# Kernel optimization log

Hardware: AMD Instinct MI355X
Metric: run time of the kernel (lower is better)

## Reference

```python
import jax, jax.numpy as jnp
import numpy as np

DN = ("NCHW", "OIHW", "NCHW")


def _conv(x, w, b, pad):
    y = jax.lax.conv_general_dilated(x, w, (1, 1), ((pad, pad), (pad, pad)), dimension_numbers=DN)
    return y + b[None, :, None, None]


def _deconv(x, w, b):
    # torch ConvTranspose2d(k=4, s=2, p=1); w: [I, O, 4, 4]
    w_eff = jnp.transpose(w, (1, 0, 2, 3))[:, :, ::-1, ::-1]  # OIHW, rot180
    y = jax.lax.conv_general_dilated(x, w_eff, (1, 1), ((2, 2), (2, 2)), lhs_dilation=(2, 2), dimension_numbers=DN)
    return y + b[None, :, None, None]


def setup_inputs() -> dict:
    key = jax.random.key(0)
    ks = jax.random.split(key, 8)
    C, Cs, H, Hs, K = 256, 768, 256, 8, 2048
    rn = lambda k, shape, scale: jax.random.normal(k, shape, jnp.float32) * scale
    return {
        "down": rn(ks[0], (1, C, H, H), 1.0),
        "swint": rn(ks[1], (1, Cs, Hs, Hs), 1.0),
        "wt_w": rn(ks[2], (C, Cs, 1, 1), 1.0 / np.sqrt(Cs)),
        "wt_b": jnp.zeros((C,), jnp.float32),
        "up_dw": rn(ks[3], (5, C, C, 4, 4), 1.0 / np.sqrt(C * 16)),
        "up_db": jnp.zeros((5, C), jnp.float32),
        "up_cw": rn(ks[4], (5, C, C, 3, 3), 1.0 / np.sqrt(C * 9)),
        "up_cb": jnp.zeros((5, C), jnp.float32),
        "gate_w": rn(ks[5], (1, C, 1, 1), 1.0 / np.sqrt(C)),
        "gate_b": jnp.zeros((1,), jnp.float32),
        "in_w": rn(ks[6], (3 * C, C), 1.0 / np.sqrt(C)),
        "in_b": jnp.zeros((3 * C,), jnp.float32),
        "out_w": rn(ks[7], (C, C), 1.0 / np.sqrt(C)),
        "out_b": jnp.zeros((C,), jnp.float32),
        "k": K,
    }


def reference(down, swint, wt_w, wt_b, up_dw, up_db, up_cw, up_cb, gate_w, gate_b, in_w, in_b, out_w, out_b, k):
    NH = 8
    B, C, H, W = down.shape  # B == 1
    s = _conv(swint, wt_w, wt_b, 0)
    for i in range(up_dw.shape[0]):
        s = _conv(jax.nn.relu(_deconv(s, up_dw[i], up_db[i])), up_cw[i], up_cb[i], 1)
    gate = jax.nn.sigmoid(_conv(down, gate_w, gate_b, 0))  # [1,1,H,W]
    down_flat = down[0].reshape(C, H * W).T  # [HW, C]
    s_flat = s[0].reshape(C, H * W).T        # [HW, C]
    _, idx = jax.lax.top_k(gate.reshape(-1), k)  # [k]
    q_in = down_flat[idx]   # [k, C]
    kv_in = s_flat[idx]     # [k, C]
    # MultiheadAttention (seq-first, batch 1)
    qw, kw, vw = in_w[:C], in_w[C:2 * C], in_w[2 * C:]
    qb, kb, vb = in_b[:C], in_b[C:2 * C], in_b[2 * C:]
    hd = C // NH
    q = (q_in @ qw.T + qb).reshape(k, NH, hd)
    kk = (kv_in @ kw.T + kb).reshape(k, NH, hd)
    v = (kv_in @ vw.T + vb).reshape(k, NH, hd)
    scores = jnp.einsum("qhd,khd->hqk", q, kk) / jnp.sqrt(jnp.asarray(hd, q.dtype))
    attn = jax.nn.softmax(scores, axis=-1)
    o = jnp.einsum("hqk,khd->qhd", attn, v).reshape(k, C)
    o = o @ out_w.T + out_b
    # scatter attended subset back into full feature map
    attended = down_flat.at[idx].set(o)
    return attended.T.reshape(B, C, H, W)
```

## Files before the change

kernel.cpp:

```cpp
#include <hip/hip_runtime.h>
#include <math.h>

#define CCH 256
#define HWP 65536
#define PCI 40

typedef short short8 __attribute__((ext_vector_type(8)));
typedef float f32x4 __attribute__((ext_vector_type(4)));
typedef unsigned short us4 __attribute__((ext_vector_type(4)));

__device__ inline unsigned short f2bf(float f) {
  unsigned u = __float_as_uint(f);
  return (unsigned short)((u + 0x7FFFu + ((u >> 16) & 1u)) >> 16);
}
__device__ inline float bf2f(unsigned short s) {
  return __uint_as_float(((unsigned)s) << 16);
}

__device__ inline void mfma_bf16(f32x4& d, short8 a, short8 b) {
  asm volatile("v_mfma_f32_16x16x32_bf16 %0, %1, %2, %0" : "+v"(d) : "v"(a), "v"(b));
}

static const size_t BUF_B_OFF = 67108864;
static const size_t TAIL_OFF  = 134217728;
static const size_t KEYS_OFF  = TAIL_OFF;
static const size_t HIST_OFF  = TAIL_OFF + 262144;
static const size_t STATE_OFF = TAIL_OFF + 263168;
static const size_t IDX_OFF   = TAIL_OFF + 263424;
static const size_t EQ_OFF    = TAIL_OFF + 271616;
static const size_t OB_OFF    = 6291456;
static const size_t WBI_OFF   = 8388608;
static const size_t WBO_OFF   = 9437184;
static const size_t SROWS_OFF = 10485760;
static const size_t DQ_OFF    = 12582912;
static const size_t GPART_OFF = 16777216;
static const size_t WT5_OFF   = 20971520;
static const size_t QB_OFF    = 31457280;
static const size_t KB_OFF    = 32505856;
static const size_t VT_OFF    = 33554432;
static const size_t CPK_OFF   = 37748736;
static const size_t DPK_OFF   = 44040192;
static const size_t WTW_OFF   = 54525952;
static const size_t WPART_OFF = 55050240;
static const size_t XQ0_OFF   = 57671680;

struct SelState { unsigned int P; int kneed; int nGreater; int nEqual; };

__global__ void k_init(unsigned int* hist, SelState* st) {
  int t = threadIdx.x;
  hist[t] = 0;
  if (t == 0) { st->P = 0u; st->kneed = 2048; st->nGreater = 0; st->nEqual = 0; }
}

__global__ void k_packall(const float* __restrict__ up_cw, const float* __restrict__ up_dw,
                          const float* __restrict__ in_w, const float* __restrict__ out_w,
                          const float* __restrict__ wt_w,
                          short* __restrict__ cpk, short* __restrict__ dpk,
                          short* __restrict__ wB5, short* __restrict__ wBi,
                          short* __restrict__ wBo, short* __restrict__ wBt) {
  int b = blockIdx.x;
  int tid = threadIdx.x;
  if (b < 1024) {
    int layer = b >> 8, co = b & 255, ci = tid;
    const float* wl = up_cw + (size_t)layer * 589824;
    short* wo = cpk + (size_t)layer * 589824;
    for (int tap = 0; tap < 9; ++tap)
      wo[((size_t)(tap * 256 + co) * 256) + ci] = (short)f2bf(wl[((size_t)(co * 256 + ci)) * 9 + tap]);
  } else if (b < 2304) {
    int bb = b - 1024;
    int layer = bb >> 8, co = bb & 255, ci = tid;
    const float* wl = up_dw + (size_t)layer * 1048576;
    for (int pq = 0; pq < 4; ++pq) {
      int p = pq >> 1, q = pq & 1;
      for (int tt = 0; tt < 4; ++tt) {
        int dyi = tt >> 1, dxi = tt & 1;
        int wr = dyi ? (1 - p) : (3 - p);
        int wc = dxi ? (1 - q) : (3 - q);
        dpk[((size_t)layer * 1048576) + ((size_t)((pq * 4 + tt) * 256 + co) * 256) + ci] =
            (short)f2bf(wl[((size_t)(ci * 256 + co)) * 16 + wr * 4 + wc]);
      }
    }
  } else if (b < 2560) {
    int co = b - 2304;
    const float* w5 = up_cw + 2359296;
    for (int kk = tid; kk < 2304; kk += 256) {
      int c = kk / 288, r = kk % 288;
      int e = r >> 5, cl = r & 31;
      wB5[(size_t)co * 2304 + kk] = (short)f2bf(w5[(size_t)co * 2304 + (size_t)(c * 32 + cl) * 9 + e]);
    }
  } else if (b < 3328) {
    int o = b - 2560;
    wBi[(size_t)o * 256 + tid] = (short)f2bf(in_w[(size_t)o * 256 + tid]);
  } else if (b < 3584) {
    int o = b - 3328;
    wBo[(size_t)o * 256 + tid] = (short)f2bf(out_w[(size_t)o * 256 + tid]);
  } else {
    int co = b - 3584;
    for (int kk = tid; kk < 768; kk += 256)
      wBt[(size_t)co * 768 + kk] = (short)f2bf(wt_w[(size_t)co * 768 + kk]);
  }
}

__global__ void k_gatecopy2(const float* __restrict__ down, const float* __restrict__ gw,
                            float* __restrict__ out, float* __restrict__ gpart) {
  int p = blockIdx.x * 256 + threadIdx.x;
  int cc = blockIdx.y;
  float acc = 0.f;
  for (int c = cc * 32; c < cc * 32 + 32; ++c) {
    float v = down[(size_t)c * HWP + p];
    out[(size_t)c * HWP + p] = v;
    acc += v * gw[c];
  }
  gpart[(size_t)cc * HWP + p] = acc;
}

__global__ void k_gkey(const float* __restrict__ gpart, unsigned* __restrict__ keys) {
  int p = blockIdx.x * 256 + threadIdx.x;
  float s = 0.f;
  for (int cc = 0; cc < 8; ++cc) s += gpart[(size_t)cc * HWP + p];
  unsigned u = __float_as_uint(s);
  keys[p] = (u & 0x80000000u) ? ~u : (u | 0x80000000u);
}

__global__ void k_hist(const unsigned int* __restrict__ keys, unsigned int* hist,
                       const SelState* st, int r) {
  __shared__ unsigned int lh[256];
  int t = threadIdx.x;
  lh[t] = 0;
  __syncthreads();
  unsigned int key = keys[blockIdx.x * 256 + t];
  bool ok = (r == 0) || ((key >> (32 - 8 * r)) == st->P);
  if (ok) atomicAdd(&lh[(key >> (24 - 8 * r)) & 255u], 1u);
  __syncthreads();
  if (lh[t]) atomicAdd(&hist[t], lh[t]);
}

__global__ void k_scan(unsigned int* hist, SelState* st) {
  if (threadIdx.x == 0) {
    int need = st->kneed;
    unsigned int cum = 0;
    for (int b = 255; b >= 0; --b) {
      unsigned int h = hist[b];
      if (cum + h >= (unsigned int)need) {
        st->P = (st->P << 8) | (unsigned int)b;
        st->kneed = need - (int)cum;
        break;
      }
      cum += h;
    }
  }
  __syncthreads();
  hist[threadIdx.x] = 0;
}

__global__ void k_compact(const unsigned int* __restrict__ keys, SelState* st,
                          int* __restrict__ idx, int* __restrict__ eq) {
  int p = blockIdx.x * 256 + threadIdx.x;
  unsigned int key = keys[p];
  unsigned int P = st->P;
  if (key > P) {
    int pos = atomicAdd(&st->nGreater, 1);
    idx[pos] = p;
  } else if (key == P) {
    int e = atomicAdd(&st->nEqual, 1);
    if (e < 4096) eq[e] = p;
  }
}

__global__ void k_finalize(SelState* st, int* idx, int* eq) {
  if (threadIdx.x != 0) return;
  int n = st->nEqual;
  if (n > 4096) n = 4096;
  for (int i = 1; i < n; ++i) {
    int v = eq[i], j = i - 1;
    while (j >= 0 && eq[j] > v) { eq[j + 1] = eq[j]; --j; }
    eq[j + 1] = v;
  }
  int g = st->nGreater;
  for (int i = 0; i < st->kneed; ++i) idx[g + i] = eq[i];
}

__global__ void k_gatherq(const float* __restrict__ down, const int* __restrict__ idx,
                          short* __restrict__ dq) {
  int j = blockIdx.x, c = threadIdx.x;
  int p = idx[j];
  dq[(size_t)j * 256 + c] = (short)f2bf(down[(size_t)c * HWP + p]);
}

__global__ __launch_bounds__(256) void k_wtconvP(const float* __restrict__ swint,
                                                 const short* __restrict__ wBt,
                                                 float* __restrict__ wpart) {
  __shared__ short x_s[64 * 40];
  int t = threadIdx.x, l = t & 63, wv = t >> 6;
  int co0 = blockIdx.x * 64;
  int ks = blockIdx.y;
  int kbase = ks * 96;
  f32x4 acc[4];
#pragma unroll
  for (int m = 0; m < 4; ++m) { f32x4 z = {0.f, 0.f, 0.f, 0.f}; acc[m] = z; }
#pragma unroll
  for (int cc = 0; cc < 3; ++cc) {
    int c0 = kbase + cc * 32;
    __syncthreads();
    {
      int ci = t >> 3, pos0 = (t & 7) * 8;
      const float* sp = swint + (size_t)(c0 + ci) * 64 + pos0;
#pragma unroll
      for (int pp = 0; pp < 8; ++pp)
        x_s[(pos0 + pp) * 40 + ci] = (short)f2bf(sp[pp]);
    }
    __syncthreads();
    short8 bfrag = *(const short8*)&x_s[(wv * 16 + (l & 15)) * 40 + (l >> 4) * 8];
#pragma unroll
    for (int m = 0; m < 4; ++m) {
      short8 af = *(const short8*)&wBt[(size_t)(co0 + m * 16 + (l & 15)) * 768 + c0 + (l >> 4) * 8];
      mfma_bf16(acc[m], af, bfrag);
    }
  }
  asm volatile("s_nop 7\n\ts_nop 7" ::);
  int pos = wv * 16 + (l & 15);
#pragma unroll
  for (int m = 0; m < 4; ++m)
#pragma unroll
    for (int r = 0; r < 4; ++r) {
      int co = co0 + m * 16 + (l >> 4) * 4 + r;
      wpart[((size_t)ks * 64 + pos) * 256 + co] = acc[m][r];
    }
}

__global__ void k_wtred(const float* __restrict__ wpart, const float* __restrict__ bias,
                        short* __restrict__ xq0) {
  int pos = blockIdx.x, co = threadIdx.x;
  float s = bias[co];
  for (int ks = 0; ks < 8; ++ks) s += wpart[((size_t)ks * 64 + pos) * 256 + co];
  xq0[(size_t)pos * 256 + co] = (short)f2bf(s);
}

__global__ __launch_bounds__(256) void k_deconv8M(const short* __restrict__ xq0,
                                                  const short* __restrict__ wpk,
                                                  const float* __restrict__ bias,
                                                  unsigned* __restrict__ yp) {
  __shared__ short x_s[121 * 260];
  int t = threadIdx.x, l = t & 63, wv = t >> 6;
  int co0 = blockIdx.x * 64;
  int pq = blockIdx.y, p = pq >> 1, q = pq & 1;
  const unsigned* xs32 = (const unsigned*)xq0;
  for (int i = t; i < 121 * 128; i += 256) {
    int row = i >> 7, c2 = i & 127;
    int iy = row / 11 - 1, ix = row % 11 - 1;
    unsigned v = 0;
    if (iy >= 0 && iy < 8 && ix >= 0 && ix < 8)
      v = xs32[(size_t)(iy * 8 + ix) * 128 + c2];
    *(unsigned*)&x_s[row * 260 + 2 * c2] = v;
  }
  __syncthreads();
  f32x4 acc[4];
#pragma unroll
  for (int m = 0; m < 4; ++m) { f32x4 z = {0.f, 0.f, 0.f, 0.f}; acc[m] = z; }
  int pos = wv * 16 + (l & 15);
  int ay = pos >> 3, bx = pos & 7;
#pragma unroll
  for (int tt = 0; tt < 4; ++tt) {
    int dyi = tt >> 1, dxi = tt & 1;
    int rowx = (ay + p + dyi) * 11 + (bx + q + dxi);
#pragma unroll
    for (int c0 = 0; c0 < 256; c0 += 32) {
      short8 bfrag = *(const short8*)&x_s[rowx * 260 + c0 + (l >> 4) * 8];
#pragma unroll
      for (int m = 0; m < 4; ++m) {
        short8 af = *(const short8*)&wpk[((size_t)((pq * 4 + tt) * 256 + co0 + m * 16 + (l & 15)) * 256) + c0 + (l >> 4) * 8];
        mfma_bf16(acc[m], af, bfrag);
      }
    }
  }
  asm volatile("s_nop 7\n\ts_nop 7" ::);
  int oy = 2 * ay + p, ox = 2 * bx + q;
#pragma unroll
  for (int m = 0; m < 4; ++m)
#pragma unroll
    for (int r4p = 0; r4p < 2; ++r4p) {
      int cob = co0 + m * 16 + (l >> 4) * 4 + 2 * r4p;
      unsigned pk = (unsigned)f2bf(fmaxf(acc[m][2 * r4p] + bias[cob], 0.f))
                  | ((unsigned)f2bf(fmaxf(acc[m][2 * r4p + 1] + bias[cob + 1], 0.f)) << 16);
      yp[(size_t)(cob >> 1) * 256 + oy * 16 + ox] = pk;
    }
}

template <int S, int O>
__global__ __launch_bounds__(256) void k_conv3u(const unsigned* __restrict__ xp,
                                                const short* __restrict__ wpk,
                                                const float* __restrict__ bias,
                                                unsigned* __restrict__ yp) {
  constexpr int WPC = (S >= 64) ? 2 : 1;
  constexpr int WCO = 4 / WPC;
  constexpr int COS = 64 / WCO;
  constexpr int MR = COS / 16;
  constexpr int PSP = S / WPC;
  constexpr int NR = PSP / 16;
  constexpr int CBK = (S + 2 + 31) / 32;
  constexpr int RS = O + 2;
  __shared__ short x_s[RS * (S + 2) * PCI];
  unsigned* x_s32 = (unsigned*)x_s;
  int t = threadIdx.x, l = t & 63, wv = t >> 6;
  int wcob = (wv % WCO) * COS;
  int wposb = (wv / WCO) * PSP;
  int row0 = blockIdx.x * O;
  int co0 = blockIdx.y * 64;
  int colb = t & 31, ci2b = t >> 5;
  f32x4 acc[O][MR][NR];
#pragma unroll
  for (int o = 0; o < O; ++o)
#pragma unroll
    for (int m = 0; m < MR; ++m)
#pragma unroll
      for (int n = 0; n < NR; ++n) { f32x4 z = {0.f, 0.f, 0.f, 0.f}; acc[o][m][n] = z; }
  for (int c0 = 0; c0 < CCH; c0 += 32) {
    int cb = c0 >> 1;
    __syncthreads();
#pragma unroll
    for (int r = 0; r < RS; ++r) {
      int gy = row0 - 1 + r;
      bool yok = (gy >= 0 && gy < S);
#pragma unroll
      for (int cbk = 0; cbk < CBK; ++cbk) {
        int col = colb + cbk * 32;
        if (col < S + 2) {
          int gx = col - 1;
          bool ok = yok && (gx >= 0) && (gx < S);
          unsigned v0 = 0, v1 = 0;
          if (ok) {
            size_t gbase = (size_t)(cb + ci2b) * S * S + (size_t)gy * S + gx;
            v0 = xp[gbase];
            v1 = xp[gbase + (size_t)8 * S * S];
          }
          int lb = (r * (S + 2) + col) * (PCI / 2);
          x_s32[lb + ci2b] = v0;
          x_s32[lb + ci2b + 8] = v1;
        }
      }
    }
    __syncthreads();
#pragma unroll
    for (int dyg = 0; dyg < 3; ++dyg)
#pragma unroll
      for (int dx = 0; dx < 3; ++dx) {
        short8 a[MR];
#pragma unroll
        for (int m = 0; m < MR; ++m)
          a[m] = *(const short8*)&wpk[((size_t)((dyg * 3 + dx) * 256 + co0 + wcob + m * 16 + (l & 15)) * 256) + c0 + (l >> 4) * 8];
#pragma unroll
        for (int o = 0; o < O; ++o) {
          short8 b[NR];
#pragma unroll
          for (int n = 0; n < NR; ++n)
            b[n] = *(const short8*)&x_s[((dyg + o) * (S + 2) + wposb + n * 16 + (l & 15) + dx) * PCI + (l >> 4) * 8];
#pragma unroll
          for (int m = 0; m < MR; ++m)
#pragma unroll
            for (int n = 0; n < NR; ++n) mfma_bf16(acc[o][m][n], a[m], b[n]);
        }
      }
  }
  asm volatile("s_nop 7\n\ts_nop 7" ::);
#pragma unroll
  for (int o = 0; o < O; ++o)
#pragma unroll
    for (int m = 0; m < MR; ++m)
#pragma unroll
      for (int n = 0; n < NR; ++n) {
        int cob = co0 + wcob + m * 16 + (l >> 4) * 4;
        int px = wposb + n * 16 + (l & 15);
#pragma unroll
        for (int r4p = 0; r4p < 2; ++r4p) {
          unsigned pk = (unsigned)f2bf(acc[o][m][n][2 * r4p] + bias[cob + 2 * r4p])
                      | ((unsigned)f2bf(acc[o][m][n][2 * r4p + 1] + bias[cob + 2 * r4p + 1]) << 16);
          yp[(size_t)((cob >> 1) + r4p) * S * S + (size_t)(row0 + o) * S + px] = pk;
        }
      }
}

__global__ __launch_bounds__(512) void k_conv3v(const unsigned* __restrict__ xp,
                                                const short* __restrict__ wpk,
                                                const float* __restrict__ bias,
                                                unsigned* __restrict__ yp) {
  constexpr int S = 128;
  constexpr int MR = 2;
  constexpr int PSP = 32;
  constexpr int NR = 2;
  __shared__ short x_s[3 * (S + 2) * PCI];
  __shared__ short w_s[9 * 64 * PCI];
  unsigned* x_s32 = (unsigned*)x_s;
  int t = threadIdx.x, l = t & 63, wv = t >> 6;
  int wcob = (wv & 1) * 32;
  int wposb = (wv >> 1) * PSP;
  int row0 = blockIdx.x;
  int co0 = blockIdx.y * 64;
  int colb = t & 31, ci2b = t >> 5;
  f32x4 acc[MR][NR];
#pragma unroll
  for (int m = 0; m < MR; ++m)
#pragma unroll
    for (int n = 0; n < NR; ++n) { f32x4 z = {0.f, 0.f, 0.f, 0.f}; acc[m][n] = z; }
  for (int c0 = 0; c0 < CCH; c0 += 32) {
    int cb = c0 >> 1;
    __syncthreads();
#pragma unroll
    for (int r = 0; r < 3; ++r) {
      int gy = row0 - 1 + r;
      bool yok = (gy >= 0 && gy < S);
#pragma unroll
      for (int cbk = 0; cbk < 5; ++cbk) {
        int col = colb + cbk * 32;
        if (col < S + 2) {
          int gx = col - 1;
          bool ok = yok && (gx >= 0) && (gx < S);
          unsigned v = 0;
          if (ok)
            v = xp[(size_t)(cb + ci2b) * S * S + (size_t)gy * S + gx];
          x_s32[(r * (S + 2) + col) * (PCI / 2) + ci2b] = v;
        }
      }
    }
    for (int i = t; i < 4608; i += 512) {
      int seg8 = i & 7;
      int rowi = i >> 3;
      int tap = rowi >> 6, co = rowi & 63;
      us4 wv4 = *(const us4*)&wpk[((size_t)(tap * 256 + co0 + co) * 256) + c0 + seg8 * 4];
      *(us4*)&w_s[rowi * PCI + seg8 * 4] = wv4;
    }
    __syncthreads();
#pragma unroll
    for (int dyg = 0; dyg < 3; ++dyg)
#pragma unroll
      for (int dx = 0; dx < 3; ++dx) {
        short8 a[MR];
#pragma unroll
        for (int m = 0; m < MR; ++m)
          a[m] = *(const short8*)&w_s[((dyg * 3 + dx) * 64 + wcob + m * 16 + (l & 15)) * PCI + (l >> 4) * 8];
        short8 b[NR];
#pragma unroll
        for (int n = 0; n < NR; ++n)
          b[n] = *(const short8*)&x_s[(dyg * (S + 2) + wposb + n * 16 + (l & 15) + dx) * PCI + (l >> 4) * 8];
#pragma unroll
        for (int m = 0; m < MR; ++m)
#pragma unroll
          for (int n = 0; n < NR; ++n) mfma_bf16(acc[m][n], a[m], b[n]);
      }
  }
  asm volatile("s_nop 7\n\ts_nop 7" ::);
#pragma unroll
  for (int m = 0; m < MR; ++m)
#pragma unroll
    for (int n = 0; n < NR; ++n) {
      int cob = co0 + wcob + m * 16 + (l >> 4) * 4;
      int px = wposb + n * 16 + (l & 15);
#pragma unroll
      for (int r4p = 0; r4p < 2; ++r4p) {
        unsigned pk = (unsigned)f2bf(acc[m][n][2 * r4p] + bias[cob + 2 * r4p])
                    | ((unsigned)f2bf(acc[m][n][2 * r4p + 1] + bias[cob + 2 * r4p + 1]) << 16);
        yp[(size_t)((cob >> 1) + r4p) * S * S + (size_t)row0 * S + px] = pk;
      }
    }
}

__global__ __launch_bounds__(512) void k_conv3v64(const unsigned* __restrict__ xp,
                                                  const short* __restrict__ wpk,
                                                  const float* __restrict__ bias,
                                                  unsigned* __restrict__ yp) {
  constexpr int S = 64;
  constexpr int MR = 2;
  __shared__ short x_s[3 * (S + 2) * PCI];
  __shared__ short w_s[9 * 64 * PCI];
  unsigned* x_s32 = (unsigned*)x_s;
  int t = threadIdx.x, l = t & 63, wv = t >> 6;
  int wcob = (wv & 1) * 32;
  int wposb = (wv >> 1) * 16;
  int row0 = blockIdx.x;
  int co0 = blockIdx.y * 64;
  int colb = t & 31, ci2b = t >> 5;
  f32x4 acc[MR];
#pragma unroll
  for (int m = 0; m < MR; ++m) { f32x4 z = {0.f, 0.f, 0.f, 0.f}; acc[m] = z; }
  for (int c0 = 0; c0 < CCH; c0 += 32) {
    int cb = c0 >> 1;
    __syncthreads();
#pragma unroll
    for (int r = 0; r < 3; ++r) {
      int gy = row0 - 1 + r;
      bool yok = (gy >= 0 && gy < S);
#pragma unroll
      for (int cbk = 0; cbk < 3; ++cbk) {
        int col = colb + cbk * 32;
        if (col < S + 2) {
          int gx = col - 1;
          bool ok = yok && (gx >= 0) && (gx < S);
          unsigned v = 0;
          if (ok)
            v = xp[(size_t)(cb + ci2b) * S * S + (size_t)gy * S + gx];
          x_s32[(r * (S + 2) + col) * (PCI / 2) + ci2b] = v;
        }
      }
    }
    for (int i = t; i < 4608; i += 512) {
      int seg8 = i & 7;
      int rowi = i >> 3;
      int tap = rowi >> 6, co = rowi & 63;
      us4 wv4 = *(const us4*)&wpk[((size_t)(tap * 256 + co0 + co) * 256) + c0 + seg8 * 4];
      *(us4*)&w_s[rowi * PCI + seg8 * 4] = wv4;
    }
    __syncthreads();
#pragma unroll
    for (int dyg = 0; dyg < 3; ++dyg)
#pragma unroll
      for (int dx = 0; dx < 3; ++dx) {
        short8 a[MR];
#pragma unroll
        for (int m = 0; m < MR; ++m)
          a[m] = *(const short8*)&w_s[((dyg * 3 + dx) * 64 + wcob + m * 16 + (l & 15)) * PCI + (l >> 4) * 8];
        short8 b = *(const short8*)&x_s[(dyg * (S + 2) + wposb + (l & 15) + dx) * PCI + (l >> 4) * 8];
#pragma unroll
        for (int m = 0; m < MR; ++m) mfma_bf16(acc[m], a[m], b);
      }
  }
  asm volatile("s_nop 7\n\ts_nop 7" ::);
#pragma unroll
  for (int m = 0; m < MR; ++m) {
    int cob = co0 + wcob + m * 16 + (l >> 4) * 4;
    int px = wposb + (l & 15);
#pragma unroll
    for (int r4p = 0; r4p < 2; ++r4p) {
      unsigned pk = (unsigned)f2bf(acc[m][2 * r4p] + bias[cob + 2 * r4p])
                  | ((unsigned)f2bf(acc[m][2 * r4p + 1] + bias[cob + 2 * r4p + 1]) << 16);
      yp[(size_t)((cob >> 1) + r4p) * S * S + (size_t)row0 * S + px] = pk;
    }
  }
}

template <int S, int O>
__global__ __launch_bounds__(256) void k_deconvu(const unsigned* __restrict__ xp,
                                                 const short* __restrict__ wpk,
                                                 const float* __restrict__ bias,
                                                 unsigned* __restrict__ yp) {
  constexpr int WPC = (S >= 64) ? 2 : 1;
  constexpr int WCO = 4 / WPC;
  constexpr int COS = 64 / WCO;
  constexpr int MR = COS / 16;
  constexpr int PSP = S / WPC;
  constexpr int NR = PSP / 16;
  constexpr int CBK = (S + 2 + 31) / 32;
  constexpr int RS = O + 1;
  const int SO = 2 * S;
  __shared__ short x_s[RS * (S + 2) * PCI];
  __shared__ short w_s[8 * 64 * PCI];
  unsigned* x_s32 = (unsigned*)x_s;
  int t = threadIdx.x, l = t & 63, wv = t >> 6;
  int wcob = (wv % WCO) * COS;
  int wposb = (wv / WCO) * PSP;
  int row0 = blockIdx.x * O;
  int co0 = blockIdx.y * 64;
  int p = blockIdx.z;
  int colb = t & 31, ci2b = t >> 5;
  f32x4 acc[2][O][MR][NR];
#pragma unroll
  for (int q = 0; q < 2; ++q)
#pragma unroll
    for (int o = 0; o < O; ++o)
#pragma unroll
      for (int m = 0; m < MR; ++m)
#pragma unroll
        for (int n = 0; n < NR; ++n) { f32x4 z = {0.f, 0.f, 0.f, 0.f}; acc[q][o][m][n] = z; }
  for (int c0 = 0; c0 < CCH; c0 += 32) {
    int cb = c0 >> 1;
    __syncthreads();
#pragma unroll
    for (int r = 0; r < RS; ++r) {
      int gy = row0 + p - 1 + r;
      bool yok = (gy >= 0 && gy < S);
#pragma unroll
      for (int cbk = 0; cbk < CBK; ++cbk) {
        int col = colb + cbk * 32;
        if (col < S + 2) {
          int gx = col - 1;
          bool ok = yok && (gx >= 0) && (gx < S);
          unsigned v0 = 0, v1 = 0;
          if (ok) {
            size_t gbase = (size_t)(cb + ci2b) * S * S + (size_t)gy * S + gx;
            v0 = xp[gbase];
            v1 = xp[gbase + (size_t)8 * S * S];
          }
          int lb = (r * (S + 2) + col) * (PCI / 2);
          x_s32[lb + ci2b] = v0;
          x_s32[lb + ci2b + 8] = v1;
        }
      }
    }
    for (int i = t; i < 4096; i += 256) {
      int seg8 = i & 7;
      int rowi = i >> 3;
      int c8 = rowi >> 6, co = rowi & 63;
      int qq = c8 >> 2, tt = c8 & 3;
      us4 wv4 = *(const us4*)&wpk[((size_t)(((2 * p + qq) * 4 + tt) * 256 + co0 + co) * 256) + c0 + seg8 * 4];
      *(us4*)&w_s[rowi * PCI + seg8 * 4] = wv4;
    }
    __syncthreads();
#pragma unroll
    for (int dyi = 0; dyi < 2; ++dyi)
#pragma unroll
      for (int o = 0; o < O; ++o) {
        short8 b[3][NR];
#pragma unroll
        for (int off = 0; off < 3; ++off)
#pragma unroll
          for (int n = 0; n < NR; ++n)
            b[off][n] = *(const short8*)&x_s[((dyi + o) * (S + 2) + wposb + n * 16 + (l & 15) + off) * PCI + (l >> 4) * 8];
#pragma unroll
        for (int q = 0; q < 2; ++q)
#pragma unroll
          for (int dxi = 0; dxi < 2; ++dxi) {
            int c8 = q * 4 + dyi * 2 + dxi;
            short8 a[MR];
#pragma unroll
            for (int m = 0; m < MR; ++m)
              a[m] = *(const short8*)&w_s[(c8 * 64 + wcob + m * 16 + (l & 15)) * PCI + (l >> 4) * 8];
#pragma unroll
            for (int m = 0; m < MR; ++m)
#pragma unroll
              for (int n = 0; n < NR; ++n) mfma_bf16(acc[q][o][m][n], a[m], b[dxi + q][n]);
          }
      }
  }
  asm volatile("s_nop 7\n\ts_nop 7" ::);
#pragma unroll
  for (int o = 0; o < O; ++o) {
    int oy = 2 * (row0 + o) + p;
#pragma unroll
    for (int m = 0; m < MR; ++m)
#pragma unroll
      for (int n = 0; n < NR; ++n) {
        int px = wposb + n * 16 + (l & 15);
#pragma unroll
        for (int r4p = 0; r4p < 2; ++r4p) {
          int cob = co0 + wcob + m * 16 + (l >> 4) * 4 + 2 * r4p;
          float b0 = bias[cob], b1 = bias[cob + 1];
          unsigned pk0 = (unsigned)f2bf(fmaxf(acc[0][o][m][n][2 * r4p] + b0, 0.f))
                       | ((unsigned)f2bf(fmaxf(acc[0][o][m][n][2 * r4p + 1] + b1, 0.f)) << 16);
          unsigned pk1 = (unsigned)f2bf(fmaxf(acc[1][o][m][n][2 * r4p] + b0, 0.f))
                       | ((unsigned)f2bf(fmaxf(acc[1][o][m][n][2 * r4p + 1] + b1, 0.f)) << 16);
          uint2 pk = make_uint2(pk0, pk1);
          *(uint2*)&yp[(size_t)(cob >> 1) * SO * SO + (size_t)oy * SO + 2 * px] = pk;
        }
      }
  }
}

__global__ __launch_bounds__(512) void k_deconvw(const unsigned* __restrict__ xp,
                                                 const short* __restrict__ wpk,
                                                 const float* __restrict__ bias,
                                                 unsigned* __restrict__ yp) {
  constexpr int S = 128;
  constexpr int O = 2;
  constexpr int MR = 2;
  constexpr int PSP = 32;
  constexpr int NR = 2;
  constexpr int RS = O + 1;
  const int SO = 2 * S;
  __shared__ short x_s[RS * (S + 2) * PCI];
  __shared__ short w_s[8 * 64 * PCI];
  unsigned* x_s32 = (unsigned*)x_s;
  int t = threadIdx.x, l = t & 63, wv = t >> 6;
  int wcob = (wv & 1) * 32;
  int wposb = (wv >> 1) * PSP;
  int row0 = blockIdx.x * O;
  int co0 = blockIdx.y * 64;
  int p = blockIdx.z;
  int colb = t & 31, ci2b = t >> 5;
  f32x4 acc[2][O][MR][NR];
#pragma unroll
  for (int q = 0; q < 2; ++q)
#pragma unroll
    for (int o = 0; o < O; ++o)
#pragma unroll
      for (int m = 0; m < MR; ++m)
#pragma unroll
        for (int n = 0; n < NR; ++n) { f32x4 z = {0.f, 0.f, 0.f, 0.f}; acc[q][o][m][n] = z; }
  for (int c0 = 0; c0 < CCH; c0 += 32) {
    int cb = c0 >> 1;
    __syncthreads();
#pragma unroll
    for (int r = 0; r < RS; ++r) {
      int gy = row0 + p - 1 + r;
      bool yok = (gy >= 0 && gy < S);
#pragma unroll
      for (int cbk = 0; cbk < 5; ++cbk) {
        int col = colb + cbk * 32;
        if (col < S + 2) {
          int gx = col - 1;
          bool ok = yok && (gx >= 0) && (gx < S);
          unsigned v = 0;
          if (ok)
            v = xp[(size_t)(cb + ci2b) * S * S + (size_t)gy * S + gx];
          x_s32[(r * (S + 2) + col) * (PCI / 2) + ci2b] = v;
        }
      }
    }
    for (int i = t; i < 4096; i += 512) {
      int seg8 = i & 7;
      int rowi = i >> 3;
      int c8 = rowi >> 6, co = rowi & 63;
      int qq = c8 >> 2, tt = c8 & 3;
      us4 wv4 = *(const us4*)&wpk[((size_t)(((2 * p + qq) * 4 + tt) * 256 + co0 + co) * 256) + c0 + seg8 * 4];
      *(us4*)&w_s[rowi * PCI + seg8 * 4] = wv4;
    }
    __syncthreads();
#pragma unroll
    for (int dyi = 0; dyi < 2; ++dyi)
#pragma unroll
      for (int o = 0; o < O; ++o) {
        short8 b[3][NR];
#pragma unroll
        for (int off = 0; off < 3; ++off)
#pragma unroll
          for (int n = 0; n < NR; ++n)
            b[off][n] = *(const short8*)&x_s[((dyi + o) * (S + 2) + wposb + n * 16 + (l & 15) + off) * PCI + (l >> 4) * 8];
#pragma unroll
        for (int q = 0; q < 2; ++q)
#pragma unroll
          for (int dxi = 0; dxi < 2; ++dxi) {
            int c8 = q * 4 + dyi * 2 + dxi;
            short8 a[MR];
#pragma unroll
            for (int m = 0; m < MR; ++m)
              a[m] = *(const short8*)&w_s[(c8 * 64 + wcob + m * 16 + (l & 15)) * PCI + (l >> 4) * 8];
#pragma unroll
            for (int m = 0; m < MR; ++m)
#pragma unroll
              for (int n = 0; n < NR; ++n) mfma_bf16(acc[q][o][m][n], a[m], b[dxi + q][n]);
          }
      }
  }
  asm volatile("s_nop 7\n\ts_nop 7" ::);
#pragma unroll
  for (int o = 0; o < O; ++o) {
    int oy = 2 * (row0 + o) + p;
#pragma unroll
    for (int m = 0; m < MR; ++m)
#pragma unroll
      for (int n = 0; n < NR; ++n) {
        int px = wposb + n * 16 + (l & 15);
#pragma unroll
        for (int r4p = 0; r4p < 2; ++r4p) {
          int cob = co0 + wcob + m * 16 + (l >> 4) * 4 + 2 * r4p;
          float b0 = bias[cob], b1 = bias[cob + 1];
          unsigned pk0 = (unsigned)f2bf(fmaxf(acc[0][o][m][n][2 * r4p] + b0, 0.f))
                       | ((unsigned)f2bf(fmaxf(acc[0][o][m][n][2 * r4p + 1] + b1, 0.f)) << 16);
          unsigned pk1 = (unsigned)f2bf(fmaxf(acc[1][o][m][n][2 * r4p] + b0, 0.f))
                       | ((unsigned)f2bf(fmaxf(acc[1][o][m][n][2 * r4p + 1] + b1, 0.f)) << 16);
          uint2 pk = make_uint2(pk0, pk1);
          *(uint2*)&yp[(size_t)(cob >> 1) * SO * SO + (size_t)oy * SO + 2 * px] = pk;
        }
      }
  }
}

__global__ __launch_bounds__(512) void k_deconvw64(const unsigned* __restrict__ xp,
                                                   const short* __restrict__ wpk,
                                                   const float* __restrict__ bias,
                                                   unsigned* __restrict__ yp) {
  constexpr int S = 64;
  constexpr int MR = 2;
  const int SO = 2 * S;
  __shared__ short x_s[2 * (S + 2) * PCI];
  __shared__ short w_s[8 * 64 * PCI];
  unsigned* x_s32 = (unsigned*)x_s;
  int t = threadIdx.x, l = t & 63, wv = t >> 6;
  int wcob = (wv & 1) * 32;
  int wposb = (wv >> 1) * 16;
  int row0 = blockIdx.x;
  int co0 = blockIdx.y * 64;
  int p = blockIdx.z;
  int colb = t & 31, ci2b = t >> 5;
  f32x4 acc[2][MR];
#pragma unroll
  for (int q = 0; q < 2; ++q)
#pragma unroll
    for (int m = 0; m < MR; ++m) { f32x4 z = {0.f, 0.f, 0.f, 0.f}; acc[q][m] = z; }
  for (int c0 = 0; c0 < CCH; c0 += 32) {
    int cb = c0 >> 1;
    __syncthreads();
#pragma unroll
    for (int r = 0; r < 2; ++r) {
      int gy = row0 + p - 1 + r;
      bool yok = (gy >= 0 && gy < S);
#pragma unroll
      for (int cbk = 0; cbk < 3; ++cbk) {
        int col = colb + cbk * 32;
        if (col < S + 2) {
          int gx = col - 1;
          bool ok = yok && (gx >= 0) && (gx < S);
          unsigned v = 0;
          if (ok)
            v = xp[(size_t)(cb + ci2b) * S * S + (size_t)gy * S + gx];
          x_s32[(r * (S + 2) + col) * (PCI / 2) + ci2b] = v;
        }
      }
    }
    for (int i = t; i < 4096; i += 512) {
      int seg8 = i & 7;
      int rowi = i >> 3;
      int c8 = rowi >> 6, co = rowi & 63;
      int qq = c8 >> 2, tt = c8 & 3;
      us4 wv4 = *(const us4*)&wpk[((size_t)(((2 * p + qq) * 4 + tt) * 256 + co0 + co) * 256) + c0 + seg8 * 4];
      *(us4*)&w_s[rowi * PCI + seg8 * 4] = wv4;
    }
    __syncthreads();
#pragma unroll
    for (int dyi = 0; dyi < 2; ++dyi) {
      short8 b[3];
#pragma unroll
      for (int off = 0; off < 3; ++off)
        b[off] = *(const short8*)&x_s[(dyi * (S + 2) + wposb + (l & 15) + off) * PCI + (l >> 4) * 8];
#pragma unroll
      for (int q = 0; q < 2; ++q)
#pragma unroll
        for (int dxi = 0; dxi < 2; ++dxi) {
          int c8 = q * 4 + dyi * 2 + dxi;
          short8 a[MR];
#pragma unroll
          for (int m = 0; m < MR; ++m)
            a[m] = *(const short8*)&w_s[(c8 * 64 + wcob + m * 16 + (l & 15)) * PCI + (l >> 4) * 8];
#pragma unroll
          for (int m = 0; m < MR; ++m) mfma_bf16(acc[q][m], a[m], b[dxi + q]);
        }
    }
  }
  asm volatile("s_nop 7\n\ts_nop 7" ::);
  int oy = 2 * row0 + p;
#pragma unroll
  for (int m = 0; m < MR; ++m) {
    int px = wposb + (l & 15);
#pragma unroll
    for (int r4p = 0; r4p < 2; ++r4p) {
      int cob = co0 + wcob + m * 16 + (l >> 4) * 4 + 2 * r4p;
      float b0 = bias[cob], b1 = bias[cob + 1];
      unsigned pk0 = (unsigned)f2bf(fmaxf(acc[0][m][2 * r4p] + b0, 0.f))
                   | ((unsigned)f2bf(fmaxf(acc[0][m][2 * r4p + 1] + b1, 0.f)) << 16);
      unsigned pk1 = (unsigned)f2bf(fmaxf(acc[1][m][2 * r4p] + b0, 0.f))
                   | ((unsigned)f2bf(fmaxf(acc[1][m][2 * r4p + 1] + b1, 0.f)) << 16);
      uint2 pk = make_uint2(pk0, pk1);
      *(uint2*)&yp[(size_t)(cob >> 1) * SO * SO + (size_t)oy * SO + 2 * px] = pk;
    }
  }
}

__global__ __launch_bounds__(256) void k_conv3sM(const unsigned* __restrict__ xp,
                                                 const short* __restrict__ wB,
                                                 const float* __restrict__ bias,
                                                 const int* __restrict__ idx,
                                                 short* __restrict__ outb) {
  __shared__ short a_s[16][296];
  __shared__ int py_s[16], px_s[16];
  int t = threadIdx.x, l = t & 63, wv = t >> 6;
  int j0 = blockIdx.x * 16;
  int co0 = blockIdx.y * 128 + wv * 32;
  if (t < 16) {
    int p = idx[j0 + t];
    py_s[t] = p >> 8;
    px_s[t] = p & 255;
  }
  f32x4 acc[2];
  { f32x4 z = {0.f, 0.f, 0.f, 0.f}; acc[0] = z; acc[1] = z; }
  for (int c = 0; c < 8; ++c) {
    __syncthreads();
    for (int i = t; i < 2304; i += 256) {
      int ci2 = i & 15;
      int je = i >> 4;
      int j = je / 9, e = je % 9;
      int gy = py_s[j] - 1 + e / 3, gx = px_s[j] - 1 + e % 3;
      unsigned v = 0;
      if (gy >= 0 && gy < 256 && gx >= 0 && gx < 256)
        v = xp[(size_t)(c * 16 + ci2) * HWP + gy * 256 + gx];
      *(unsigned*)&a_s[j][e * 32 + 2 * ci2] = v;
    }
    __syncthreads();
#pragma unroll
    for (int s = 0; s < 9; ++s) {
      short8 a = *(const short8*)&a_s[l & 15][s * 32 + (l >> 4) * 8];
      int kg = c * 288 + s * 32 + (l >> 4) * 8;
      short8 b0 = *(const short8*)&wB[(size_t)(co0 + (l & 15)) * 2304 + kg];
      short8 b1 = *(const short8*)&wB[(size_t)(co0 + 16 + (l & 15)) * 2304 + kg];
      mfma_bf16(acc[0], a, b0);
      mfma_bf16(acc[1], a, b1);
    }
  }
  asm volatile("s_nop 7\n\ts_nop 7" ::);
#pragma unroll
  for (int n = 0; n < 2; ++n)
#pragma unroll
    for (int r = 0; r < 4; ++r) {
      int j = j0 + (l >> 4) * 4 + r;
      int co = co0 + n * 16 + (l & 15);
      outb[(size_t)j * 256 + co] = (short)f2bf(acc[n][r] + bias[co]);
    }
}

__global__ __launch_bounds__(256) void k_qkv3(const short* __restrict__ dq,
                                              const short* __restrict__ sr,
                                              const short* __restrict__ wBi,
                                              const float* __restrict__ bias,
                                              short* __restrict__ Qb,
                                              short* __restrict__ Kb,
                                              short* __restrict__ Vt) {
  __shared__ short a_s[16 * 264];
  unsigned* a_s32 = (unsigned*)a_s;
  int t = threadIdx.x, l = t & 63, wv = t >> 6;
  int j0 = blockIdx.x * 16;
  int third = blockIdx.y >> 2;
  const unsigned* s32 = (const unsigned*)(third ? sr : dq);
  for (int i = t; i < 2048; i += 256) {
    int row = i >> 7, c2 = i & 127;
    a_s32[row * 132 + c2] = s32[(size_t)(j0 + row) * 128 + c2];
  }
  __syncthreads();
  int cog = blockIdx.y * 64 + wv * 16 + (l & 15);
  f32x4 acc = {0.f, 0.f, 0.f, 0.f};
  const short* brow = wBi + (size_t)cog * 256 + (l >> 4) * 8;
  const short* arow = a_s + (l & 15) * 264 + (l >> 4) * 8;
#pragma unroll
  for (int kc = 0; kc < 8; ++kc) {
    short8 a = *(const short8*)(arow + kc * 32);
    short8 b = *(const short8*)(brow + kc * 32);
    mfma_bf16(acc, a, b);
  }
  asm volatile("s_nop 7\n\ts_nop 7" ::);
  float bv = bias[cog];
  int co = cog & 255;
  int h = co >> 5, d = co & 31;
#pragma unroll
  for (int r = 0; r < 4; ++r) {
    int j = j0 + (l >> 4) * 4 + r;
    short v = (short)f2bf(acc[r] + bv);
    if (third == 0)      Qb[((size_t)h * 2048 + j) * 32 + d] = v;
    else if (third == 1) Kb[((size_t)h * 2048 + j) * 32 + d] = v;
    else                 Vt[((size_t)h * 32 + d) * 2048 + j] = v;
  }
}

__global__ __launch_bounds__(256) void k_fattn(const short* __restrict__ Qb,
                                               const short* __restrict__ Kb,
                                               const short* __restrict__ Vt,
                                               short* __restrict__ Ob) {
  __shared__ short P_lds[4][16][136];
  int t = threadIdx.x, l = t & 63, wv = t >> 6;
  int h = blockIdx.y;
  int q0 = blockIdx.x * 64 + wv * 16;
  const short* Qh = Qb + (size_t)h * 2048 * 32;
  const short* Kh = Kb + (size_t)h * 2048 * 32;
  const short* Vh = Vt + (size_t)h * 32 * 2048;
  short8 a_q = *(const short8*)&Qh[(size_t)(q0 + (l & 15)) * 32 + (l >> 4) * 8];
  f32x4 o0 = {0.f, 0.f, 0.f, 0.f}, o1 = {0.f, 0.f, 0.f, 0.f};
  float m_run[4], l_run[4];
#pragma unroll
  for (int r = 0; r < 4; ++r) { m_run[r] = -3e38f; l_run[r] = 0.f; }
  const float scale = 0.17677669529663687f;
  for (int k0 = 0; k0 < 2048; k0 += 128) {
    f32x4 s[8];
#pragma unroll
    for (int kt = 0; kt < 8; ++kt) {
      f32x4 z = {0.f, 0.f, 0.f, 0.f};
      s[kt] = z;
      short8 b = *(const short8*)&Kh[(size_t)(k0 + kt * 16 + (l & 15)) * 32 + (l >> 4) * 8];
      mfma_bf16(s[kt], a_q, b);
    }
    asm volatile("s_nop 7\n\ts_nop 7" ::);
    float tm[4];
#pragma unroll
    for (int r = 0; r < 4; ++r) {
      float mx = s[0][r];
#pragma unroll
      for (int kt = 1; kt < 8; ++kt) mx = fmaxf(mx, s[kt][r]);
      tm[r] = mx * scale;
    }
#pragma unroll
    for (int mask = 1; mask < 16; mask <<= 1)
#pragma unroll
      for (int r = 0; r < 4; ++r) tm[r] = fmaxf(tm[r], __shfl_xor(tm[r], mask));
    float mn[4], al[4], rs[4];
#pragma unroll
    for (int r = 0; r < 4; ++r) {
      mn[r] = fmaxf(m_run[r], tm[r]);
      al[r] = __expf(m_run[r] - mn[r]);
      rs[r] = 0.f;
    }
#pragma unroll
    for (int kt = 0; kt < 8; ++kt)
#pragma unroll
      for (int r = 0; r < 4; ++r) {
        float pv = __expf(s[kt][r] * scale - mn[r]);
        s[kt][r] = pv;
        rs[r] += pv;
      }
#pragma unroll
    for (int mask = 1; mask < 16; mask <<= 1)
#pragma unroll
      for (int r = 0; r < 4; ++r) rs[r] += __shfl_xor(rs[r], mask);
#pragma unroll
    for (int r = 0; r < 4; ++r) {
      l_run[r] = l_run[r] * al[r] + rs[r];
      m_run[r] = mn[r];
      o0[r] *= al[r];
      o1[r] *= al[r];
    }
#pragma unroll
    for (int kt = 0; kt < 8; ++kt)
#pragma unroll
      for (int r = 0; r < 4; ++r)
        P_lds[wv][(l >> 4) * 4 + r][kt * 16 + (l & 15)] = (short)f2bf(s[kt][r]);
#pragma unroll
    for (int kc = 0; kc < 4; ++kc) {
      short8 ap = *(const short8*)&P_lds[wv][l & 15][kc * 32 + (l >> 4) * 8];
      short8 b0 = *(const short8*)&Vh[(size_t)(l & 15) * 2048 + k0 + kc * 32 + (l >> 4) * 8];
      short8 b1 = *(const short8*)&Vh[(size_t)(16 + (l & 15)) * 2048 + k0 + kc * 32 + (l >> 4) * 8];
      mfma_bf16(o0, ap, b0);
      mfma_bf16(o1, ap, b1);
    }
  }
  asm volatile("s_nop 7\n\ts_nop 7" ::);
#pragma unroll
  for (int r = 0; r < 4; ++r) {
    float inv = 1.f / l_run[r];
    int qr = q0 + (l >> 4) * 4 + r;
    Ob[(size_t)qr * 256 + h * 32 + (l & 15)] = (short)f2bf(o0[r] * inv);
    Ob[(size_t)qr * 256 + h * 32 + 16 + (l & 15)] = (short)f2bf(o1[r] * inv);
  }
}

__global__ __launch_bounds__(256) void k_outprojM(const short* __restrict__ Ob,
                                                  const short* __restrict__ wBo,
                                                  const float* __restrict__ ob,
                                                  const int* __restrict__ idx,
                                                  float* __restrict__ out) {
  __shared__ short a_s[16 * 264];
  __shared__ int jp[16];
  unsigned* a_s32 = (unsigned*)a_s;
  const unsigned* s32 = (const unsigned*)Ob;
  int t = threadIdx.x, l = t & 63, wv = t >> 6;
  int j0 = blockIdx.x * 16;
  if (t < 16) jp[t] = idx[j0 + t];
  for (int i = t; i < 2048; i += 256) {
    int row = i >> 7, c2 = i & 127;
    a_s32[row * 132 + c2] = s32[(size_t)(j0 + row) * 128 + c2];
  }
  __syncthreads();
  int co = blockIdx.y * 64 + wv * 16 + (l & 15);
  f32x4 acc = {0.f, 0.f, 0.f, 0.f};
  const short* brow = wBo + (size_t)co * 256 + (l >> 4) * 8;
  const short* arow = a_s + (l & 15) * 264 + (l >> 4) * 8;
#pragma unroll
  for (int kc = 0; kc < 8; ++kc) {
    short8 a = *(const short8*)(arow + kc * 32);
    short8 b = *(const short8*)(brow + kc * 32);
    mfma_bf16(acc, a, b);
  }
  asm volatile("s_nop 7\n\ts_nop 7" ::);
  float bv = ob[co];
#pragma unroll
  for (int r = 0; r < 4; ++r) {
    int jl = (l >> 4) * 4 + r;
    out[(size_t)co * HWP + jp[jl]] = acc[r] + bv;
  }
}

extern "C" void kernel_launch(void* const* d_in, const int* in_sizes, int n_in,
                              void* d_out, int out_size, void* d_ws, size_t ws_size,
                              hipStream_t stream) {
  const float* down  = (const float*)d_in[0];
  const float* swint = (const float*)d_in[1];
  const float* wt_w  = (const float*)d_in[2];
  const float* wt_b  = (const float*)d_in[3];
  const float* up_dw = (const float*)d_in[4];
  const float* up_db = (const float*)d_in[5];
  const float* up_cw = (const float*)d_in[6];
  const float* up_cb = (const float*)d_in[7];
  const float* gate_w = (const float*)d_in[8];
  const float* in_w  = (const float*)d_in[10];
  const float* in_b  = (const float*)d_in[11];
  const float* out_w = (const float*)d_in[12];
  const float* out_b = (const float*)d_in[13];
  float* out = (float*)d_out;
  char* ws = (char*)d_ws;

  unsigned* actA = (unsigned*)ws;
  unsigned* actB = (unsigned*)(ws + BUF_B_OFF);
  unsigned int* keys = (unsigned int*)(ws + KEYS_OFF);
  unsigned int* hist = (unsigned int*)(ws + HIST_OFF);
  SelState* st = (SelState*)(ws + STATE_OFF);
  int* idx = (int*)(ws + IDX_OFF);
  int* eq = (int*)(ws + EQ_OFF);
  short* Ob = (short*)(ws + OB_OFF);
  short* wBi = (short*)(ws + WBI_OFF);
  short* wBo = (short*)(ws + WBO_OFF);
  short* srowsb = (short*)(ws + SROWS_OFF);
  short* dq = (short*)(ws + DQ_OFF);
  float* gpart = (float*)(ws + GPART_OFF);
  short* wB5 = (short*)(ws + WT5_OFF);
  short* Qb = (short*)(ws + QB_OFF);
  short* Kb = (short*)(ws + KB_OFF);
  short* Vt = (short*)(ws + VT_OFF);
  short* cpk = (short*)(ws + CPK_OFF);
  short* dpk = (short*)(ws + DPK_OFF);
  short* wBt = (short*)(ws + WTW_OFF);
  float* wpart = (float*)(ws + WPART_OFF);
  short* xq0 = (short*)(ws + XQ0_OFF);

  k_init<<<1, 256, 0, stream>>>(hist, st);

  k_gatecopy2<<<dim3(256, 8), 256, 0, stream>>>(down, gate_w, out, gpart);
  k_gkey<<<256, 256, 0, stream>>>(gpart, keys);
  for (int r = 0; r < 4; ++r) {
    k_hist<<<256, 256, 0, stream>>>(keys, hist, st, r);
    k_scan<<<1, 256, 0, stream>>>(hist, st);
  }
  k_compact<<<256, 256, 0, stream>>>(keys, st, idx, eq);
  k_finalize<<<1, 64, 0, stream>>>(st, idx, eq);

  k_gatherq<<<2048, 256, 0, stream>>>(down, idx, dq);

  k_packall<<<3840, 256, 0, stream>>>(up_cw, up_dw, in_w, out_w, wt_w,
                                      cpk, dpk, wB5, wBi, wBo, wBt);

  k_wtconvP<<<dim3(4, 8), 256, 0, stream>>>(swint, wBt, wpart);
  k_wtred<<<64, 256, 0, stream>>>(wpart, wt_b, xq0);
  k_deconv8M<<<dim3(4, 4), 256, 0, stream>>>(xq0, dpk, up_db, actB);

  k_conv3u<16, 2><<<dim3(8, 4), 256, 0, stream>>>(actB, cpk, up_cb, actA);
  k_deconvu<16, 2><<<dim3(8, 4, 2), 256, 0, stream>>>(actA, dpk + 1048576, up_db + 256, actB);
  k_conv3u<32, 2><<<dim3(16, 4), 256, 0, stream>>>(actB, cpk + 589824, up_cb + 256, actA);
  k_deconvu<32, 2><<<dim3(16, 4, 2), 256, 0, stream>>>(actA, dpk + 2 * 1048576, up_db + 512, actB);
  k_conv3v64<<<dim3(64, 4), 512, 0, stream>>>(actB, cpk + 2 * 589824, up_cb + 512, actA);
  k_deconvw64<<<dim3(64, 4, 2), 512, 0, stream>>>(actA, dpk + 3 * 1048576, up_db + 768, actB);
  k_conv3v<<<dim3(128, 4), 512, 0, stream>>>(actB, cpk + 3 * 589824, up_cb + 768, actA);
  k_deconvw<<<dim3(64, 4, 2), 512, 0, stream>>>(actA, dpk + 4 * 1048576, up_db + 1024, actB);

  k_conv3sM<<<dim3(128, 2), 256, 0, stream>>>(actB, wB5, up_cb + 1024, idx, srowsb);

  k_qkv3<<<dim3(128, 12), 256, 0, stream>>>(dq, srowsb, wBi, in_b, Qb, Kb, Vt);
  k_fattn<<<dim3(32, 8), 256, 0, stream>>>(Qb, Kb, Vt, Ob);
  k_outprojM<<<dim3(128, 4), 256, 0, stream>>>(Ob, wBo, out_b, idx, out);
}
```

Before: 627.4 us.

## Fuse top-k radix select and gather into one cooperative kernel

```diff
diff --git a/kernel.cpp b/kernel.cpp
--- a/kernel.cpp
+++ b/kernel.cpp
@@ -1,5 +1,8 @@
 #include <hip/hip_runtime.h>
+#include <hip/hip_cooperative_groups.h>
 #include <math.h>
+
+namespace cg = cooperative_groups;
 
 #define CCH 256
 #define HWP 65536
@@ -45,12 +48,6 @@
 static const size_t XQ0_OFF   = 57671680;
 
 struct SelState { unsigned int P; int kneed; int nGreater; int nEqual; };
-
-__global__ void k_init(unsigned int* hist, SelState* st) {
-  int t = threadIdx.x;
-  hist[t] = 0;
-  if (t == 0) { st->P = 0u; st->kneed = 2048; st->nGreater = 0; st->nEqual = 0; }
-}
 
 __global__ void k_packall(const float* __restrict__ up_cw, const float* __restrict__ up_dw,
                           const float* __restrict__ in_w, const float* __restrict__ out_w,
@@ -114,77 +111,83 @@
   gpart[(size_t)cc * HWP + p] = acc;
 }
 
-__global__ void k_gkey(const float* __restrict__ gpart, unsigned* __restrict__ keys) {
-  int p = blockIdx.x * 256 + threadIdx.x;
+__global__ __launch_bounds__(256) void k_topk(const float* __restrict__ gpart,
+                                              const float* __restrict__ down,
+                                              unsigned* __restrict__ hist,
+                                              SelState* st,
+                                              int* __restrict__ idx,
+                                              int* __restrict__ eq,
+                                              short* __restrict__ dq) {
+  cg::grid_group grid = cg::this_grid();
+  int t = threadIdx.x;
+  int p = blockIdx.x * 256 + t;
   float s = 0.f;
   for (int cc = 0; cc < 8; ++cc) s += gpart[(size_t)cc * HWP + p];
   unsigned u = __float_as_uint(s);
-  keys[p] = (u & 0x80000000u) ? ~u : (u | 0x80000000u);
-}
-
-__global__ void k_hist(const unsigned int* __restrict__ keys, unsigned int* hist,
-                       const SelState* st, int r) {
-  __shared__ unsigned int lh[256];
-  int t = threadIdx.x;
-  lh[t] = 0;
-  __syncthreads();
-  unsigned int key = keys[blockIdx.x * 256 + t];
-  bool ok = (r == 0) || ((key >> (32 - 8 * r)) == st->P);
-  if (ok) atomicAdd(&lh[(key >> (24 - 8 * r)) & 255u], 1u);
-  __syncthreads();
-  if (lh[t]) atomicAdd(&hist[t], lh[t]);
-}
-
-__global__ void k_scan(unsigned int* hist, SelState* st) {
-  if (threadIdx.x == 0) {
-    int need = st->kneed;
-    unsigned int cum = 0;
-    for (int b = 255; b >= 0; --b) {
-      unsigned int h = hist[b];
-      if (cum + h >= (unsigned int)need) {
-        st->P = (st->P << 8) | (unsigned int)b;
-        st->kneed = need - (int)cum;
-        break;
-      }
-      cum += h;
-    }
-  }
-  __syncthreads();
-  hist[threadIdx.x] = 0;
-}
-
-__global__ void k_compact(const unsigned int* __restrict__ keys, SelState* st,
-                          int* __restrict__ idx, int* __restrict__ eq) {
-  int p = blockIdx.x * 256 + threadIdx.x;
-  unsigned int key = keys[p];
-  unsigned int P = st->P;
-  if (key > P) {
-    int pos = atomicAdd(&st->nGreater, 1);
-    idx[pos] = p;
-  } else if (key == P) {
-    int e = atomicAdd(&st->nEqual, 1);
-    if (e < 4096) eq[e] = p;
-  }
-}
-
-__global__ void k_finalize(SelState* st, int* idx, int* eq) {
-  if (threadIdx.x != 0) return;
-  int n = st->nEqual;
-  if (n > 4096) n = 4096;
-  for (int i = 1; i < n; ++i) {
-    int v = eq[i], j = i - 1;
-    while (j >= 0 && eq[j] > v) { eq[j + 1] = eq[j]; --j; }
-    eq[j + 1] = v;
-  }
-  int g = st->nGreater;
-  for (int i = 0; i < st->kneed; ++i) idx[g + i] = eq[i];
-}
-
-__global__ void k_gatherq(const float* __restrict__ down, const int* __restrict__ idx,
-                          short* __restrict__ dq) {
-  int j = blockIdx.x, c = threadIdx.x;
-  int p = idx[j];
-  dq[(size_t)j * 256 + c] = (short)f2bf(down[(size_t)c * HWP + p]);
+  unsigned key = (u & 0x80000000u) ? ~u : (u | 0x80000000u);
+  if (blockIdx.x == 0) {
+    hist[t] = 0;
+    if (t == 0) { st->P = 0u; st->kneed = 2048; st->nGreater = 0; st->nEqual = 0; }
+  }
+  grid.sync();
+  __shared__ unsigned lh[256];
+  for (int r = 0; r < 4; ++r) {
+    lh[t] = 0;
+    __syncthreads();
+    unsigned P = st->P;
+    bool ok = (r == 0) || ((key >> (32 - 8 * r)) == P);
+    if (ok) atomicAdd(&lh[(key >> (24 - 8 * r)) & 255u], 1u);
+    __syncthreads();
+    if (lh[t]) atomicAdd(&hist[t], lh[t]);
+    grid.sync();
+    if (blockIdx.x == 0) {
+      if (t == 0) {
+        int need = st->kneed;
+        unsigned cum = 0;
+        for (int b = 255; b >= 0; --b) {
+          unsigned h = hist[b];
+          if (cum + h >= (unsigned)need) {
+            st->P = (st->P << 8) | (unsigned)b;
+            st->kneed = need - (int)cum;
+            break;
+          }
+          cum += h;
+        }
+      }
+      __syncthreads();
+      hist[t] = 0;
+    }
+    grid.sync();
+  }
+  {
+    unsigned P = st->P;
+    if (key > P) {
+      int pos = atomicAdd(&st->nGreater, 1);
+      idx[pos] = p;
+    } else if (key == P) {
+      int e = atomicAdd(&st->nEqual, 1);
+      if (e < 4096) eq[e] = p;
+    }
+  }
+  grid.sync();
+  if (blockIdx.x == 0 && t == 0) {
+    int n = st->nEqual;
+    if (n > 4096) n = 4096;
+    for (int i = 1; i < n; ++i) {
+      int v = eq[i], j = i - 1;
+      while (j >= 0 && eq[j] > v) { eq[j + 1] = eq[j]; --j; }
+      eq[j + 1] = v;
+    }
+    int g = st->nGreater;
+    for (int i = 0; i < st->kneed; ++i) idx[g + i] = eq[i];
+  }
+  grid.sync();
+#pragma unroll
+  for (int jj = 0; jj < 8; ++jj) {
+    int j = blockIdx.x * 8 + jj;
+    int pj = idx[j];
+    dq[(size_t)j * 256 + t] = (short)f2bf(down[(size_t)t * HWP + pj]);
+  }
 }
 
 __global__ __launch_bounds__(256) void k_wtconvP(const float* __restrict__ swint,
@@ -1091,7 +1094,6 @@
 
   unsigned* actA = (unsigned*)ws;
   unsigned* actB = (unsigned*)(ws + BUF_B_OFF);
-  unsigned int* keys = (unsigned int*)(ws + KEYS_OFF);
   unsigned int* hist = (unsigned int*)(ws + HIST_OFF);
   SelState* st = (SelState*)(ws + STATE_OFF);
   int* idx = (int*)(ws + IDX_OFF);
@@ -1112,18 +1114,13 @@
   float* wpart = (float*)(ws + WPART_OFF);
   short* xq0 = (short*)(ws + XQ0_OFF);
 
-  k_init<<<1, 256, 0, stream>>>(hist, st);
-
   k_gatecopy2<<<dim3(256, 8), 256, 0, stream>>>(down, gate_w, out, gpart);
-  k_gkey<<<256, 256, 0, stream>>>(gpart, keys);
-  for (int r = 0; r < 4; ++r) {
-    k_hist<<<256, 256, 0, stream>>>(keys, hist, st, r);
-    k_scan<<<1, 256, 0, stream>>>(hist, st);
-  }
-  k_compact<<<256, 256, 0, stream>>>(keys, st, idx, eq);
-  k_finalize<<<1, 64, 0, stream>>>(st, idx, eq);
-
-  k_gatherq<<<2048, 256, 0, stream>>>(down, idx, dq);
+
+  {
+    void* args[] = {(void*)&gpart, (void*)&down, (void*)&hist, (void*)&st,
+                    (void*)&idx, (void*)&eq, (void*)&dq};
+    hipLaunchCooperativeKernel(k_topk, dim3(256), dim3(256), args, 0u, stream);
+  }
 
   k_packall<<<3840, 256, 0, stream>>>(up_cw, up_dw, in_w, out_w, wt_w,
                                       cpk, dpk, wB5, wBi, wBo, wBt);
```

Measured after the change: 869.1 us. +38.5%, slower.

## Fuse radix top-k selection into a single-block kernel

Applied to the files above, without the earlier changes.

```diff
diff --git a/kernel.cpp b/kernel.cpp
--- a/kernel.cpp
+++ b/kernel.cpp
@@ -24,8 +24,6 @@
 static const size_t BUF_B_OFF = 67108864;
 static const size_t TAIL_OFF  = 134217728;
 static const size_t KEYS_OFF  = TAIL_OFF;
-static const size_t HIST_OFF  = TAIL_OFF + 262144;
-static const size_t STATE_OFF = TAIL_OFF + 263168;
 static const size_t IDX_OFF   = TAIL_OFF + 263424;
 static const size_t EQ_OFF    = TAIL_OFF + 271616;
 static const size_t OB_OFF    = 6291456;
@@ -43,14 +41,6 @@
 static const size_t WTW_OFF   = 54525952;
 static const size_t WPART_OFF = 55050240;
 static const size_t XQ0_OFF   = 57671680;
-
-struct SelState { unsigned int P; int kneed; int nGreater; int nEqual; };
-
-__global__ void k_init(unsigned int* hist, SelState* st) {
-  int t = threadIdx.x;
-  hist[t] = 0;
-  if (t == 0) { st->P = 0u; st->kneed = 2048; st->nGreater = 0; st->nEqual = 0; }
-}
 
 __global__ void k_packall(const float* __restrict__ up_cw, const float* __restrict__ up_dw,
                           const float* __restrict__ in_w, const float* __restrict__ out_w,
@@ -122,62 +112,69 @@
   keys[p] = (u & 0x80000000u) ? ~u : (u | 0x80000000u);
 }
 
-__global__ void k_hist(const unsigned int* __restrict__ keys, unsigned int* hist,
-                       const SelState* st, int r) {
-  __shared__ unsigned int lh[256];
+__global__ __launch_bounds__(1024) void k_select1(const unsigned* __restrict__ keys,
+                                                  int* __restrict__ idx,
+                                                  int* __restrict__ eq) {
+  __shared__ unsigned lh[256];
+  __shared__ unsigned sP;
+  __shared__ int skneed, snG, snE;
   int t = threadIdx.x;
-  lh[t] = 0;
+  unsigned key[64];
+#pragma unroll
+  for (int i = 0; i < 64; ++i) key[i] = keys[i * 1024 + t];
+  if (t == 0) { sP = 0u; skneed = 2048; snG = 0; snE = 0; }
   __syncthreads();
-  unsigned int key = keys[blockIdx.x * 256 + t];
-  bool ok = (r == 0) || ((key >> (32 - 8 * r)) == st->P);
-  if (ok) atomicAdd(&lh[(key >> (24 - 8 * r)) & 255u], 1u);
+  for (int r = 0; r < 4; ++r) {
+    if (t < 256) lh[t] = 0;
+    __syncthreads();
+    unsigned P = sP;
+#pragma unroll
+    for (int i = 0; i < 64; ++i) {
+      bool ok = (r == 0) || ((key[i] >> (32 - 8 * r)) == P);
+      if (ok) atomicAdd(&lh[(key[i] >> (24 - 8 * r)) & 255u], 1u);
+    }
+    __syncthreads();
+    if (t == 0) {
+      int need = skneed;
+      unsigned cum = 0;
+      for (int b = 255; b >= 0; --b) {
+        unsigned h = lh[b];
+        if (cum + h >= (unsigned)need) {
+          sP = (sP << 8) | (unsigned)b;
+          skneed = need - (int)cum;
+          break;
+        }
+        cum += h;
+      }
+    }
+    __syncthreads();
+  }
+  {
+    unsigned P = sP;
+#pragma unroll
+    for (int i = 0; i < 64; ++i) {
+      int p = i * 1024 + t;
+      if (key[i] > P) {
+        int pos = atomicAdd(&snG, 1);
+        idx[pos] = p;
+      } else if (key[i] == P) {
+        int e = atomicAdd(&snE, 1);
+        if (e < 4096) eq[e] = p;
+      }
+    }
+  }
   __syncthreads();
-  if (lh[t]) atomicAdd(&hist[t], lh[t]);
-}
-
-__global__ void k_scan(unsigned int* hist, SelState* st) {
-  if (threadIdx.x == 0) {
-    int need = st->kneed;
-    unsigned int cum = 0;
-    for (int b = 255; b >= 0; --b) {
-      unsigned int h = hist[b];
-      if (cum + h >= (unsigned int)need) {
-        st->P = (st->P << 8) | (unsigned int)b;
-        st->kneed = need - (int)cum;
-        break;
-      }
-      cum += h;
-    }
-  }
-  __syncthreads();
-  hist[threadIdx.x] = 0;
-}
-
-__global__ void k_compact(const unsigned int* __restrict__ keys, SelState* st,
-                          int* __restrict__ idx, int* __restrict__ eq) {
-  int p = blockIdx.x * 256 + threadIdx.x;
-  unsigned int key = keys[p];
-  unsigned int P = st->P;
-  if (key > P) {
-    int pos = atomicAdd(&st->nGreater, 1);
-    idx[pos] = p;
-  } else if (key == P) {
-    int e = atomicAdd(&st->nEqual, 1);
-    if (e < 4096) eq[e] = p;
-  }
-}
-
-__global__ void k_finalize(SelState* st, int* idx, int* eq) {
-  if (threadIdx.x != 0) return;
-  int n = st->nEqual;
-  if (n > 4096) n = 4096;
-  for (int i = 1; i < n; ++i) {
-    int v = eq[i], j = i - 1;
-    while (j >= 0 && eq[j] > v) { eq[j + 1] = eq[j]; --j; }
-    eq[j + 1] = v;
-  }
-  int g = st->nGreater;
-  for (int i = 0; i < st->kneed; ++i) idx[g + i] = eq[i];
+  if (t == 0) {
+    int n = snE;
+    if (n > 4096) n = 4096;
+    for (int i = 1; i < n; ++i) {
+      int v = eq[i], j = i - 1;
+      while (j >= 0 && eq[j] > v) { eq[j + 1] = eq[j]; --j; }
+      eq[j + 1] = v;
+    }
+    int g = snG;
+    for (int i = 0; i < skneed; ++i) idx[g + i] = eq[i];
+  }
 }
 
 __global__ void k_gatherq(const float* __restrict__ down, const int* __restrict__ idx,
@@ -1092,8 +1089,6 @@
   unsigned* actA = (unsigned*)ws;
   unsigned* actB = (unsigned*)(ws + BUF_B_OFF);
   unsigned int* keys = (unsigned int*)(ws + KEYS_OFF);
-  unsigned int* hist = (unsigned int*)(ws + HIST_OFF);
-  SelState* st = (SelState*)(ws + STATE_OFF);
   int* idx = (int*)(ws + IDX_OFF);
   int* eq = (int*)(ws + EQ_OFF);
   short* Ob = (short*)(ws + OB_OFF);
@@ -1112,17 +1107,9 @@
   float* wpart = (float*)(ws + WPART_OFF);
   short* xq0 = (short*)(ws + XQ0_OFF);
 
-  k_init<<<1, 256, 0, stream>>>(hist, st);
-
   k_gatecopy2<<<dim3(256, 8), 256, 0, stream>>>(down, gate_w, out, gpart);
   k_gkey<<<256, 256, 0, stream>>>(gpart, keys);
-  for (int r = 0; r < 4; ++r) {
-    k_hist<<<256, 256, 0, stream>>>(keys, hist, st, r);
-    k_scan<<<1, 256, 0, stream>>>(hist, st);
-  }
-  k_compact<<<256, 256, 0, stream>>>(keys, st, idx, eq);
-  k_finalize<<<1, 64, 0, stream>>>(st, idx, eq);
-
+  k_select1<<<1, 1024, 0, stream>>>(keys, idx, eq);
   k_gatherq<<<2048, 256, 0, stream>>>(down, idx, dq);
 
   k_packall<<<3840, 256, 0, stream>>>(up_cw, up_dw, in_w, out_w, wt_w,
```

Result: no change. 626.9 us (-0.1%).
